# Performance work log

Hardware: AMD Instinct MI355X
Metric: run time of the kernel (lower is better)

Reference implementation:

```python
import jax, jax.numpy as jnp
import numpy as np


def setup_inputs() -> dict:
    key = jax.random.key(0)
    k1, k2, k3, k4 = jax.random.split(key, 4)
    n, C, t, h, w = 1, 256, 8, 64, 64
    heads = 8
    S = t + h + w - 2  # 134 axial positions per query
    attention = jax.random.normal(k1, (n, heads * S, t, h, w), dtype=jnp.float32)
    value = jax.random.normal(k2, (n, C, t, h, w), dtype=jnp.float32)
    conv_w = jax.random.normal(k3, (C, C), dtype=jnp.float32) / np.float32(np.sqrt(C))
    conv_b = jax.random.normal(k4, (C,), dtype=jnp.float32)
    return {"attention": attention, "value": value, "conv_w": conv_w,
            "conv_b": conv_b, "num_heads": heads}


def _grid_attn_map(A, V):
    """Criss-cross axial attention aggregation.
    A: [b, t+h+w-2, t, h, w] per-query weights over the t-axis (t entries,
       self included), h-axis (h-1 entries, self excluded) and w-axis
       (w-1 entries, self excluded).
    V: [b, c, t, h, w]. Returns [b, c, t, h, w].
    """
    b, c, t, h, w = V.shape
    A_t = A[:, :t]                  # [b, t, t, h, w]
    A_h = A[:, t:t + h - 1]         # [b, h-1, t, h, w]
    A_w = A[:, t + h - 1:]          # [b, w-1, t, h, w]

    # t-axis (self included): sum over key frame s
    out = jnp.einsum('bsthw,bcshw->bcthw', A_t, V)

    # h-axis (self excluded): channel j addresses key row p = j + (j >= q).
    # Build dense [h] channel axis with a zero at p == q via a padded gather.
    zpad = jnp.zeros((b, 1, t, h, w), A.dtype)
    A_h_pad = jnp.concatenate([A_h, zpad], axis=1)  # channel h-1 is zero
    p = jnp.arange(h)[:, None]
    q = jnp.arange(h)[None, :]
    inv_h = jnp.where(p < q, p, jnp.where(p == q, h - 1, p - 1))  # [h(p), h(q)]
    A_h_full = jnp.take_along_axis(A_h_pad, inv_h[None, :, None, :, None], axis=1)  # [b,p,t,q,w]
    out = out + jnp.einsum('bptqw,bctpw->bctqw', A_h_full, V)

    # w-axis (self excluded), same trick along w
    A_w_pad = jnp.concatenate([A_w, zpad], axis=1)  # channel w-1 is zero (h==w here OK; recompute pad generally)
    pw = jnp.arange(w)[:, None]
    qw = jnp.arange(w)[None, :]
    inv_w = jnp.where(pw < qw, pw, jnp.where(pw == qw, w - 1, pw - 1))  # [w(p), w(q)]
    A_w_full = jnp.take_along_axis(A_w_pad, inv_w[None, :, None, None, :], axis=1)  # [b,p,t,h,q]
    out = out + jnp.einsum('bpthq,bcthp->bcthq', A_w_full, V)
    return out


def reference(attention, value, conv_w, conv_b, num_heads):
    n, C, t, h, w = value.shape
    S = t + h + w - 2
    # 1x1x1 Conv3d == per-position channel matmul
    pv = jnp.einsum('ncthw,oc->nothw', value, conv_w) + conv_b[None, :, None, None, None]
    pv = pv.reshape(n * num_heads, C // num_heads, t, h, w)
    A = attention.reshape(n * num_heads, S, t, h, w)
    out = _grid_attn_map(A, pv)
    return out.reshape(n, num_heads, C // num_heads, t, h, w)
```

## Files before the change

### kernel.cpp

```cpp
#include <hip/hip_runtime.h>

#define SS   134
#define HWP  4096
#define THW  32768

typedef float f32x4 __attribute__((ext_vector_type(4)));
typedef short bf16x8 __attribute__((ext_vector_type(8)));
typedef short bf16x4 __attribute__((ext_vector_type(4)));

__device__ __forceinline__ unsigned short f2bf(float f) {
  unsigned int u = __float_as_uint(f);
  u += 0x7fff + ((u >> 16) & 1);
  return (unsigned short)(u >> 16);
}

__global__ __launch_bounds__(256) void w2bf(const float* __restrict__ W,
                                            unsigned short* __restrict__ Wbf) {
  const int i = (blockIdx.x * 256 + threadIdx.x) * 4;
  const float4 w4 = *(const float4*)&W[i];
  bf16x4 b;
  b.x = (short)f2bf(w4.x);
  b.y = (short)f2bf(w4.y);
  b.z = (short)f2bf(w4.z);
  b.w = (short)f2bf(w4.w);
  *(bf16x4*)&Wbf[i] = b;
}

__global__ __launch_bounds__(512) void conv1x1_v4(
    const float* __restrict__ V, const unsigned short* __restrict__ Wbf,
    const float* __restrict__ bias, float* __restrict__ PV) {
  __shared__ unsigned short sW[256 * 260];
  __shared__ unsigned short sV[2][128 * 40];
  const int tid = threadIdx.x;
  const int x0 = blockIdx.x * 128;
  const int lane = tid & 63;
  const int wv = tid >> 6;
  const int m = lane & 15;
  const int q = lane >> 4;

  {
    const int o = tid >> 1;
    const int half = (tid & 1) * 128;
#pragma unroll
    for (int r = 0; r < 16; ++r)
      *(bf16x8*)&sW[o * 260 + half + r * 8] =
          *(const bf16x8*)&Wbf[o * 256 + half + r * 8];
  }

  const int c_s = tid >> 4;
  const int x8 = (tid & 15) * 8;
  const float* __restrict__ vstage = V + (size_t)c_s * THW + x0 + x8;

  {
    const float4 va = *(const float4*)&vstage[0];
    const float4 vb = *(const float4*)&vstage[4];
    sV[0][(x8 + 0) * 40 + c_s] = f2bf(va.x);
    sV[0][(x8 + 1) * 40 + c_s] = f2bf(va.y);
    sV[0][(x8 + 2) * 40 + c_s] = f2bf(va.z);
    sV[0][(x8 + 3) * 40 + c_s] = f2bf(va.w);
    sV[0][(x8 + 4) * 40 + c_s] = f2bf(vb.x);
    sV[0][(x8 + 5) * 40 + c_s] = f2bf(vb.y);
    sV[0][(x8 + 6) * 40 + c_s] = f2bf(vb.z);
    sV[0][(x8 + 7) * 40 + c_s] = f2bf(vb.w);
  }
  __syncthreads();

  f32x4 acc[2][8];
#pragma unroll
  for (int i = 0; i < 2; ++i)
#pragma unroll
    for (int j = 0; j < 8; ++j)
      acc[i][j] = (f32x4){0.f, 0.f, 0.f, 0.f};

  for (int kk = 0; kk < 8; ++kk) {
    const int cur = kk & 1;
    float4 pva, pvb;
    if (kk < 7) {
      pva = *(const float4*)&vstage[(size_t)(kk + 1) * 32 * THW];
      pvb = *(const float4*)&vstage[(size_t)(kk + 1) * 32 * THW + 4];
    }
    bf16x8 fa[2], fb[8];
#pragma unroll
    for (int i = 0; i < 2; ++i)
      fa[i] = *(const bf16x8*)&sW[(wv * 32 + i * 16 + m) * 260 + kk * 32 + q * 8];
#pragma unroll
    for (int j = 0; j < 8; ++j)
      fb[j] = *(const bf16x8*)&sV[cur][(j * 16 + m) * 40 + q * 8];
#pragma unroll
    for (int i = 0; i < 2; ++i)
#pragma unroll
      for (int j = 0; j < 8; ++j)
        acc[i][j] = __builtin_amdgcn_mfma_f32_16x16x32_bf16(fa[i], fb[j], acc[i][j], 0, 0, 0);
    if (kk < 7) {
      const int nb = cur ^ 1;
      sV[nb][(x8 + 0) * 40 + c_s] = f2bf(pva.x);
      sV[nb][(x8 + 1) * 40 + c_s] = f2bf(pva.y);
      sV[nb][(x8 + 2) * 40 + c_s] = f2bf(pva.z);
      sV[nb][(x8 + 3) * 40 + c_s] = f2bf(pva.w);
      sV[nb][(x8 + 4) * 40 + c_s] = f2bf(pvb.x);
      sV[nb][(x8 + 5) * 40 + c_s] = f2bf(pvb.y);
      sV[nb][(x8 + 6) * 40 + c_s] = f2bf(pvb.z);
      sV[nb][(x8 + 7) * 40 + c_s] = f2bf(pvb.w);
    }
    __syncthreads();
  }

#pragma unroll
  for (int i = 0; i < 2; ++i) {
#pragma unroll
    for (int r = 0; r < 4; ++r) {
      const int o = wv * 32 + i * 16 + q * 4 + r;
      const float bo = bias[o];
#pragma unroll
      for (int j = 0; j < 8; ++j)
        PV[(size_t)o * THW + x0 + j * 16 + m] = acc[i][j][r] + bo;
    }
  }
}

__global__ __launch_bounds__(256) void attn_t(
    const float* __restrict__ A, const float* __restrict__ PV,
    float* __restrict__ O) {
  const int b = blockIdx.x;
  const int hd = b & 7;
  const int cb = (b >> 3) & 3;
  const int xt = b >> 5;
  const int tid = threadIdx.x;
  const int xi = xt * 128 + (tid & 31) * 4;
  const int c = cb * 8 + (tid >> 5);

  const float* __restrict__ At = A + (size_t)hd * SS * THW + xi;
  const size_t pvh = (size_t)hd * 32 * THW;
  const float* __restrict__ pvc = PV + pvh + (size_t)c * THW + xi;

  f32x4 acc[8];
#pragma unroll
  for (int t = 0; t < 8; ++t) acc[t] = (f32x4){0.f, 0.f, 0.f, 0.f};

  for (int s = 0; s < 8; ++s) {
    const f32x4 pvv = *(const f32x4*)&pvc[(size_t)s * HWP];
#pragma unroll
    for (int t = 0; t < 8; ++t) {
      const f32x4 a = *(const f32x4*)&At[(size_t)s * THW + (size_t)t * HWP];
      acc[t] += a * pvv;
    }
  }

#pragma unroll
  for (int t = 0; t < 8; ++t)
    *(f32x4*)&O[pvh + (size_t)c * THW + (size_t)t * HWP + xi] = acc[t];
}

__global__ __launch_bounds__(512) void attn_h(
    const float* __restrict__ A, const float* __restrict__ PV,
    float* __restrict__ O) {
  const int b = blockIdx.x;
  const int hd = b & 7;
  const int chb = (b >> 3) & 1;
  const int qb = (b >> 4) & 3;
  const int tq = b >> 6;
  const int tid = threadIdx.x;
  const int lane = tid & 63;
  const int wv = tid >> 6;
  const int w4 = (lane & 15) * 4;
  const int cl = lane >> 4;
  const int q0 = qb * 16 + wv * 2;
  const int c0 = chb * 16;

  __shared__ float slab[2][4 * 16 * 64];

  const float* __restrict__ Ab = A + (size_t)hd * SS * THW + (size_t)tq * HWP;
  const size_t pvh = (size_t)hd * 32 * THW;
  const float* __restrict__ PVh = PV + pvh;

  f32x4 acc[2][4];
#pragma unroll
  for (int qi = 0; qi < 2; ++qi) {
    const int q = q0 + qi;
#pragma unroll
    for (int g = 0; g < 4; ++g) {
      const int c = c0 + g * 4 + cl;
      acc[qi][g] =
          *(const f32x4*)&O[pvh + (size_t)c * THW + (size_t)tq * HWP + q * 64 + w4];
    }
  }

  const int w4s = (tid & 15) * 4;
  const int c_s = (tid >> 4) & 15;
  const int pp0 = tid >> 8;
  const float* __restrict__ pvstage =
      PVh + (size_t)(c0 + c_s) * THW + (size_t)tq * HWP + w4s;
  const int sbase = c_s * 64 + w4s;

  f32x4 stg[2];
#pragma unroll
  for (int r = 0; r < 2; ++r)
    stg[r] = *(const f32x4*)&pvstage[(pp0 + 2 * r) * 64];
#pragma unroll
  for (int r = 0; r < 2; ++r)
    *(f32x4*)&slab[0][(pp0 + 2 * r) * 1024 + sbase] = stg[r];
  __syncthreads();

  for (int ck = 0; ck < 16; ++ck) {
    const int cur = ck & 1;
    if (ck < 15) {
#pragma unroll
      for (int r = 0; r < 2; ++r)
        stg[r] = *(const f32x4*)&pvstage[((ck + 1) * 4 + pp0 + 2 * r) * 64];
    }
#pragma unroll
    for (int pp = 0; pp < 4; ++pp) {
      const int p = ck * 4 + pp;
      f32x4 a[2];
#pragma unroll
      for (int qi = 0; qi < 2; ++qi) {
        const int q = q0 + qi;
        const int row = p - (q < p ? 1 : 0);
        f32x4 av = *(const f32x4*)&Ab[(size_t)(8 + row) * THW + q * 64 + w4];
        if (q == p) av = (f32x4){0.f, 0.f, 0.f, 0.f};
        a[qi] = av;
      }
      f32x4 v[4];
#pragma unroll
      for (int g = 0; g < 4; ++g)
        v[g] = *(const f32x4*)&slab[cur][pp * 1024 + (g * 4 + cl) * 64 + w4];
#pragma unroll
      for (int qi = 0; qi < 2; ++qi)
#pragma unroll
        for (int g = 0; g < 4; ++g)
          acc[qi][g] += a[qi] * v[g];
    }
    if (ck < 15) {
#pragma unroll
      for (int r = 0; r < 2; ++r)
        *(f32x4*)&slab[cur ^ 1][(pp0 + 2 * r) * 1024 + sbase] = stg[r];
    }
    __syncthreads();
  }

#pragma unroll
  for (int qi = 0; qi < 2; ++qi) {
    const int q = q0 + qi;
#pragma unroll
    for (int g = 0; g < 4; ++g) {
      const int c = c0 + g * 4 + cl;
      *(f32x4*)&O[pvh + (size_t)c * THW + (size_t)tq * HWP + q * 64 + w4] =
          acc[qi][g];
    }
  }
}

__global__ __launch_bounds__(256) void attn_w(
    const float* __restrict__ A, const float* __restrict__ PV,
    float* __restrict__ O) {
  const int b = blockIdx.x;
  const int hb = b & 15;
  const int tq = (b >> 4) & 7;
  const int hd = b >> 7;
  const int tid = threadIdx.x;
  const int wq = tid & 63;
  const int cg = tid >> 6;
  const int h0 = hb * 4;

  __shared__ float slab[32 * 64 * 4];

  const float* __restrict__ Ab = A + (size_t)hd * SS * THW + (size_t)tq * HWP;
  const size_t pvh = (size_t)hd * 32 * THW;

#pragma unroll 4
  for (int i = 0; i < 8; ++i) {
    const int fid = tid + i * 256;
    const int w4s = (fid & 15) * 4;
    const int h = (fid >> 4) & 3;
    const int c = fid >> 6;
    const f32x4 v =
        *(const f32x4*)&PV[pvh + (size_t)c * THW + (size_t)tq * HWP + (h0 + h) * 64 + w4s];
    slab[(c * 64 + w4s + 0) * 4 + h] = v.x;
    slab[(c * 64 + w4s + 1) * 4 + h] = v.y;
    slab[(c * 64 + w4s + 2) * 4 + h] = v.z;
    slab[(c * 64 + w4s + 3) * 4 + h] = v.w;
  }

  f32x4 racc[8];
#pragma unroll
  for (int ci = 0; ci < 8; ++ci) {
    const int c = cg + ci * 4;
    f32x4 r;
#pragma unroll
    for (int hh = 0; hh < 4; ++hh)
      r[hh] = O[pvh + (size_t)c * THW + (size_t)tq * HWP + (h0 + hh) * 64 + wq];
    racc[ci] = r;
  }
  __syncthreads();

#pragma unroll 4
  for (int p = 0; p < 64; ++p) {
    const int row = 71 + p - (wq <= p ? 1 : 0);
    const float* pa = Ab + (size_t)row * THW + h0 * 64 + wq;
    f32x4 a;
    a.x = pa[0];
    a.y = pa[64];
    a.z = pa[128];
    a.w = pa[192];
    if (p == wq) a = (f32x4){0.f, 0.f, 0.f, 0.f};
#pragma unroll
    for (int ci = 0; ci < 8; ++ci) {
      const f32x4 v = *(const f32x4*)&slab[(cg + ci * 4) * 256 + p * 4];
      racc[ci] += a * v;
    }
  }

#pragma unroll
  for (int ci = 0; ci < 8; ++ci) {
    const int c = cg + ci * 4;
#pragma unroll
    for (int hh = 0; hh < 4; ++hh)
      O[pvh + (size_t)c * THW + (size_t)tq * HWP + (h0 + hh) * 64 + wq] = racc[ci][hh];
  }
}

extern "C" void kernel_launch(void* const* d_in, const int* in_sizes, int n_in,
                              void* d_out, int out_size, void* d_ws, size_t ws_size,
                              hipStream_t stream) {
  const float* A = (const float*)d_in[0];
  const float* V = (const float*)d_in[1];
  const float* W = (const float*)d_in[2];
  const float* bias = (const float*)d_in[3];
  float* out = (float*)d_out;
  float* pv = (float*)d_ws;

  unsigned short* Wbf = (unsigned short*)d_out;

  w2bf<<<dim3(64), 256, 0, stream>>>(W, Wbf);
  conv1x1_v4<<<dim3(256), 512, 0, stream>>>(V, Wbf, bias, pv);
  attn_t<<<dim3(1024), 256, 0, stream>>>(A, pv, out);
  attn_h<<<dim3(512), 512, 0, stream>>>(A, pv, out);
  attn_w<<<dim3(1024), 256, 0, stream>>>(A, pv, out);
}
```

Before: 326.9 us.

## Fuse t-axis attention into h-axis kernel and split w-kernel channels

Removes the separate attn_t kernel and folds the t-axis accumulation into the h-axis kernel, which now starts from zero instead of reloading partial output. This removes one launch and a full write-then-read round trip of the output tensor. The w-axis kernel is also split into two channel halves per block, which doubles the grid and halves the shared slab and register accumulators. The cost is that each half re-reads the same w-axis attention weights, doubling that traffic unless it hits in cache.

New measurement: 362.8 us. 1.11x slower.

```diff
diff --git a/kernel.cpp b/kernel.cpp
--- a/kernel.cpp
+++ b/kernel.cpp
@@ -118,40 +118,7 @@
   }
 }
 
-__global__ __launch_bounds__(256) void attn_t(
-    const float* __restrict__ A, const float* __restrict__ PV,
-    float* __restrict__ O) {
-  const int b = blockIdx.x;
-  const int hd = b & 7;
-  const int cb = (b >> 3) & 3;
-  const int xt = b >> 5;
-  const int tid = threadIdx.x;
-  const int xi = xt * 128 + (tid & 31) * 4;
-  const int c = cb * 8 + (tid >> 5);
-
-  const float* __restrict__ At = A + (size_t)hd * SS * THW + xi;
-  const size_t pvh = (size_t)hd * 32 * THW;
-  const float* __restrict__ pvc = PV + pvh + (size_t)c * THW + xi;
-
-  f32x4 acc[8];
-#pragma unroll
-  for (int t = 0; t < 8; ++t) acc[t] = (f32x4){0.f, 0.f, 0.f, 0.f};
-
-  for (int s = 0; s < 8; ++s) {
-    const f32x4 pvv = *(const f32x4*)&pvc[(size_t)s * HWP];
-#pragma unroll
-    for (int t = 0; t < 8; ++t) {
-      const f32x4 a = *(const f32x4*)&At[(size_t)s * THW + (size_t)t * HWP];
-      acc[t] += a * pvv;
-    }
-  }
-
-#pragma unroll
-  for (int t = 0; t < 8; ++t)
-    *(f32x4*)&O[pvh + (size_t)c * THW + (size_t)t * HWP + xi] = acc[t];
-}
-
-__global__ __launch_bounds__(512) void attn_h(
+__global__ __launch_bounds__(512) void attn_th2(
     const float* __restrict__ A, const float* __restrict__ PV,
     float* __restrict__ O) {
   const int b = blockIdx.x;
@@ -175,15 +142,10 @@
 
   f32x4 acc[2][4];
 #pragma unroll
-  for (int qi = 0; qi < 2; ++qi) {
-    const int q = q0 + qi;
-#pragma unroll
-    for (int g = 0; g < 4; ++g) {
-      const int c = c0 + g * 4 + cl;
-      acc[qi][g] =
-          *(const f32x4*)&O[pvh + (size_t)c * THW + (size_t)tq * HWP + q * 64 + w4];
-    }
-  }
+  for (int qi = 0; qi < 2; ++qi)
+#pragma unroll
+    for (int g = 0; g < 4; ++g)
+      acc[qi][g] = (f32x4){0.f, 0.f, 0.f, 0.f};
 
   const int w4s = (tid & 15) * 4;
   const int c_s = (tid >> 4) & 15;
@@ -196,6 +158,22 @@
 #pragma unroll
   for (int r = 0; r < 2; ++r)
     stg[r] = *(const f32x4*)&pvstage[(pp0 + 2 * r) * 64];
+
+  for (int s = 0; s < 8; ++s) {
+#pragma unroll
+    for (int qi = 0; qi < 2; ++qi) {
+      const int q = q0 + qi;
+      const f32x4 a = *(const f32x4*)&Ab[(size_t)s * THW + q * 64 + w4];
+#pragma unroll
+      for (int g = 0; g < 4; ++g) {
+        const int c = c0 + g * 4 + cl;
+        const f32x4 v =
+            *(const f32x4*)&PVh[(size_t)c * THW + (size_t)s * HWP + q * 64 + w4];
+        acc[qi][g] += a * v;
+      }
+    }
+  }
+
 #pragma unroll
   for (int r = 0; r < 2; ++r)
     *(f32x4*)&slab[0][(pp0 + 2 * r) * 1024 + sbase] = stg[r];
@@ -255,36 +233,38 @@
     float* __restrict__ O) {
   const int b = blockIdx.x;
   const int hb = b & 15;
-  const int tq = (b >> 4) & 7;
-  const int hd = b >> 7;
+  const int cw = (b >> 4) & 1;
+  const int tq = (b >> 5) & 7;
+  const int hd = b >> 8;
   const int tid = threadIdx.x;
   const int wq = tid & 63;
   const int cg = tid >> 6;
   const int h0 = hb * 4;
-
-  __shared__ float slab[32 * 64 * 4];
+  const int c0 = cw * 16;
+
+  __shared__ float slab[16 * 64 * 4];
 
   const float* __restrict__ Ab = A + (size_t)hd * SS * THW + (size_t)tq * HWP;
   const size_t pvh = (size_t)hd * 32 * THW;
 
-#pragma unroll 4
-  for (int i = 0; i < 8; ++i) {
+#pragma unroll
+  for (int i = 0; i < 4; ++i) {
     const int fid = tid + i * 256;
     const int w4s = (fid & 15) * 4;
     const int h = (fid >> 4) & 3;
     const int c = fid >> 6;
     const f32x4 v =
-        *(const f32x4*)&PV[pvh + (size_t)c * THW + (size_t)tq * HWP + (h0 + h) * 64 + w4s];
+        *(const f32x4*)&PV[pvh + (size_t)(c0 + c) * THW + (size_t)tq * HWP + (h0 + h) * 64 + w4s];
     slab[(c * 64 + w4s + 0) * 4 + h] = v.x;
     slab[(c * 64 + w4s + 1) * 4 + h] = v.y;
     slab[(c * 64 + w4s + 2) * 4 + h] = v.z;
     slab[(c * 64 + w4s + 3) * 4 + h] = v.w;
   }
 
-  f32x4 racc[8];
-#pragma unroll
-  for (int ci = 0; ci < 8; ++ci) {
-    const int c = cg + ci * 4;
+  f32x4 racc[4];
+#pragma unroll
+  for (int ci = 0; ci < 4; ++ci) {
+    const int c = c0 + cg + ci * 4;
     f32x4 r;
 #pragma unroll
     for (int hh = 0; hh < 4; ++hh)
@@ -304,15 +284,15 @@
     a.w = pa[192];
     if (p == wq) a = (f32x4){0.f, 0.f, 0.f, 0.f};
 #pragma unroll
-    for (int ci = 0; ci < 8; ++ci) {
+    for (int ci = 0; ci < 4; ++ci) {
       const f32x4 v = *(const f32x4*)&slab[(cg + ci * 4) * 256 + p * 4];
       racc[ci] += a * v;
     }
   }
 
 #pragma unroll
-  for (int ci = 0; ci < 8; ++ci) {
-    const int c = cg + ci * 4;
+  for (int ci = 0; ci < 4; ++ci) {
+    const int c = c0 + cg + ci * 4;
 #pragma unroll
     for (int hh = 0; hh < 4; ++hh)
       O[pvh + (size_t)c * THW + (size_t)tq * HWP + (h0 + hh) * 64 + wq] = racc[ci][hh];
@@ -333,7 +313,6 @@
 
   w2bf<<<dim3(64), 256, 0, stream>>>(W, Wbf);
   conv1x1_v4<<<dim3(256), 512, 0, stream>>>(V, Wbf, bias, pv);
-  attn_t<<<dim3(1024), 256, 0, stream>>>(A, pv, out);
-  attn_h<<<dim3(512), 512, 0, stream>>>(A, pv, out);
-  attn_w<<<dim3(1024), 256, 0, stream>>>(A, pv, out);
-}
+  attn_th2<<<dim3(512), 512, 0, stream>>>(A, pv, out);
+  attn_w<<<dim3(2048), 256, 0, stream>>>(A, pv, out);
+}
```

## Pre-convert V to bf16 in a fused cast kernel and split attn_w over channels

Applied to the files above, without the earlier changes.

A single cast kernel now converts both V and W to bf16, writing them into the output buffer as scratch. The conv kernel then loads 8 bf16 values per thread instead of converting fp32 in its inner loop. Separately, attn_w is split into two channel halves, doubling its grid and halving its shared slab and register accumulators to raise occupancy. The cost is an extra full pass over V in memory, and every attn_w block now re-reads its attention rows once per channel half.

Measured after the change: 347.4 us. +6.3%, slower.

```diff
diff --git a/kernel.cpp b/kernel.cpp
--- a/kernel.cpp
+++ b/kernel.cpp
@@ -14,20 +14,33 @@
   return (unsigned short)(u >> 16);
 }
 
-__global__ __launch_bounds__(256) void w2bf(const float* __restrict__ W,
-                                            unsigned short* __restrict__ Wbf) {
-  const int i = (blockIdx.x * 256 + threadIdx.x) * 4;
-  const float4 w4 = *(const float4*)&W[i];
-  bf16x4 b;
-  b.x = (short)f2bf(w4.x);
-  b.y = (short)f2bf(w4.y);
-  b.z = (short)f2bf(w4.z);
-  b.w = (short)f2bf(w4.w);
-  *(bf16x4*)&Wbf[i] = b;
-}
-
-__global__ __launch_bounds__(512) void conv1x1_v4(
-    const float* __restrict__ V, const unsigned short* __restrict__ Wbf,
+__global__ __launch_bounds__(256) void inputs_bf(
+    const float* __restrict__ V, const float* __restrict__ W,
+    unsigned short* __restrict__ Vbf, unsigned short* __restrict__ Wbf) {
+  const int b = blockIdx.x;
+  if (b < 8192) {
+    const int i = b * 1024 + threadIdx.x * 4;
+    const float4 v4 = *(const float4*)&V[i];
+    bf16x4 o;
+    o.x = (short)f2bf(v4.x);
+    o.y = (short)f2bf(v4.y);
+    o.z = (short)f2bf(v4.z);
+    o.w = (short)f2bf(v4.w);
+    *(bf16x4*)&Vbf[i] = o;
+  } else {
+    const int i = (b - 8192) * 1024 + threadIdx.x * 4;
+    const float4 w4 = *(const float4*)&W[i];
+    bf16x4 o;
+    o.x = (short)f2bf(w4.x);
+    o.y = (short)f2bf(w4.y);
+    o.z = (short)f2bf(w4.z);
+    o.w = (short)f2bf(w4.w);
+    *(bf16x4*)&Wbf[i] = o;
+  }
+}
+
+__global__ __launch_bounds__(512) void conv1x1_v5(
+    const unsigned short* __restrict__ Vbf, const unsigned short* __restrict__ Wbf,
     const float* __restrict__ bias, float* __restrict__ PV) {
   __shared__ unsigned short sW[256 * 260];
   __shared__ unsigned short sV[2][128 * 40];
@@ -49,19 +62,13 @@
 
   const int c_s = tid >> 4;
   const int x8 = (tid & 15) * 8;
-  const float* __restrict__ vstage = V + (size_t)c_s * THW + x0 + x8;
+  const unsigned short* __restrict__ vstage = Vbf + (size_t)c_s * THW + x0 + x8;
 
   {
-    const float4 va = *(const float4*)&vstage[0];
-    const float4 vb = *(const float4*)&vstage[4];
-    sV[0][(x8 + 0) * 40 + c_s] = f2bf(va.x);
-    sV[0][(x8 + 1) * 40 + c_s] = f2bf(va.y);
-    sV[0][(x8 + 2) * 40 + c_s] = f2bf(va.z);
-    sV[0][(x8 + 3) * 40 + c_s] = f2bf(va.w);
-    sV[0][(x8 + 4) * 40 + c_s] = f2bf(vb.x);
-    sV[0][(x8 + 5) * 40 + c_s] = f2bf(vb.y);
-    sV[0][(x8 + 6) * 40 + c_s] = f2bf(vb.z);
-    sV[0][(x8 + 7) * 40 + c_s] = f2bf(vb.w);
+    const bf16x8 v8 = *(const bf16x8*)&vstage[0];
+#pragma unroll
+    for (int e = 0; e < 8; ++e)
+      sV[0][(x8 + e) * 40 + c_s] = (unsigned short)v8[e];
   }
   __syncthreads();
 
@@ -74,10 +81,9 @@
 
   for (int kk = 0; kk < 8; ++kk) {
     const int cur = kk & 1;
-    float4 pva, pvb;
+    bf16x8 pv8;
     if (kk < 7) {
-      pva = *(const float4*)&vstage[(size_t)(kk + 1) * 32 * THW];
-      pvb = *(const float4*)&vstage[(size_t)(kk + 1) * 32 * THW + 4];
+      pv8 = *(const bf16x8*)&vstage[(size_t)(kk + 1) * 32 * THW];
     }
     bf16x8 fa[2], fb[8];
 #pragma unroll
@@ -93,14 +99,9 @@
         acc[i][j] = __builtin_amdgcn_mfma_f32_16x16x32_bf16(fa[i], fb[j], acc[i][j], 0, 0, 0);
     if (kk < 7) {
       const int nb = cur ^ 1;
-      sV[nb][(x8 + 0) * 40 + c_s] = f2bf(pva.x);
-      sV[nb][(x8 + 1) * 40 + c_s] = f2bf(pva.y);
-      sV[nb][(x8 + 2) * 40 + c_s] = f2bf(pva.z);
-      sV[nb][(x8 + 3) * 40 + c_s] = f2bf(pva.w);
-      sV[nb][(x8 + 4) * 40 + c_s] = f2bf(pvb.x);
-      sV[nb][(x8 + 5) * 40 + c_s] = f2bf(pvb.y);
-      sV[nb][(x8 + 6) * 40 + c_s] = f2bf(pvb.z);
-      sV[nb][(x8 + 7) * 40 + c_s] = f2bf(pvb.w);
+#pragma unroll
+      for (int e = 0; e < 8; ++e)
+        sV[nb][(x8 + e) * 40 + c_s] = (unsigned short)pv8[e];
     }
     __syncthreads();
   }
@@ -255,36 +256,38 @@
     float* __restrict__ O) {
   const int b = blockIdx.x;
   const int hb = b & 15;
-  const int tq = (b >> 4) & 7;
-  const int hd = b >> 7;
+  const int cw = (b >> 4) & 1;
+  const int tq = (b >> 5) & 7;
+  const int hd = b >> 8;
   const int tid = threadIdx.x;
   const int wq = tid & 63;
   const int cg = tid >> 6;
   const int h0 = hb * 4;
-
-  __shared__ float slab[32 * 64 * 4];
+  const int c0 = cw * 16;
+
+  __shared__ float slab[16 * 64 * 4];
 
   const float* __restrict__ Ab = A + (size_t)hd * SS * THW + (size_t)tq * HWP;
   const size_t pvh = (size_t)hd * 32 * THW;
 
-#pragma unroll 4
-  for (int i = 0; i < 8; ++i) {
+#pragma unroll
+  for (int i = 0; i < 4; ++i) {
     const int fid = tid + i * 256;
     const int w4s = (fid & 15) * 4;
     const int h = (fid >> 4) & 3;
     const int c = fid >> 6;
     const f32x4 v =
-        *(const f32x4*)&PV[pvh + (size_t)c * THW + (size_t)tq * HWP + (h0 + h) * 64 + w4s];
+        *(const f32x4*)&PV[pvh + (size_t)(c0 + c) * THW + (size_t)tq * HWP + (h0 + h) * 64 + w4s];
     slab[(c * 64 + w4s + 0) * 4 + h] = v.x;
     slab[(c * 64 + w4s + 1) * 4 + h] = v.y;
     slab[(c * 64 + w4s + 2) * 4 + h] = v.z;
     slab[(c * 64 + w4s + 3) * 4 + h] = v.w;
   }
 
-  f32x4 racc[8];
-#pragma unroll
-  for (int ci = 0; ci < 8; ++ci) {
-    const int c = cg + ci * 4;
+  f32x4 racc[4];
+#pragma unroll
+  for (int ci = 0; ci < 4; ++ci) {
+    const int c = c0 + cg + ci * 4;
     f32x4 r;
 #pragma unroll
     for (int hh = 0; hh < 4; ++hh)
@@ -304,15 +307,15 @@
     a.w = pa[192];
     if (p == wq) a = (f32x4){0.f, 0.f, 0.f, 0.f};
 #pragma unroll
-    for (int ci = 0; ci < 8; ++ci) {
+    for (int ci = 0; ci < 4; ++ci) {
       const f32x4 v = *(const f32x4*)&slab[(cg + ci * 4) * 256 + p * 4];
       racc[ci] += a * v;
     }
   }
 
 #pragma unroll
-  for (int ci = 0; ci < 8; ++ci) {
-    const int c = cg + ci * 4;
+  for (int ci = 0; ci < 4; ++ci) {
+    const int c = c0 + cg + ci * 4;
 #pragma unroll
     for (int hh = 0; hh < 4; ++hh)
       O[pvh + (size_t)c * THW + (size_t)tq * HWP + (h0 + hh) * 64 + wq] = racc[ci][hh];
@@ -329,11 +332,12 @@
   float* out = (float*)d_out;
   float* pv = (float*)d_ws;
 
-  unsigned short* Wbf = (unsigned short*)d_out;
-
-  w2bf<<<dim3(64), 256, 0, stream>>>(W, Wbf);
-  conv1x1_v4<<<dim3(256), 512, 0, stream>>>(V, Wbf, bias, pv);
+  unsigned short* Vbf = (unsigned short*)d_out;
+  unsigned short* Wbf = Vbf + (size_t)8 * 1024 * 1024;
+
+  inputs_bf<<<dim3(8256), 256, 0, stream>>>(V, W, Vbf, Wbf);
+  conv1x1_v5<<<dim3(256), 512, 0, stream>>>(Vbf, Wbf, bias, pv);
   attn_t<<<dim3(1024), 256, 0, stream>>>(A, pv, out);
   attn_h<<<dim3(512), 512, 0, stream>>>(A, pv, out);
-  attn_w<<<dim3(1024), 256, 0, stream>>>(A, pv, out);
-}
+  attn_w<<<dim3(2048), 256, 0, stream>>>(A, pv, out);
+}
```

## Fuse t-axis aggregation into w-axis kernel and drop separate attn_t pass

Applied to the files above, without the earlier changes.

The t-axis einsum is folded into the w-axis kernel. Each block first accumulates the t contribution in registers, using the same spatial tile it already owns, then adds the w-axis terms from its shared-memory PV slab. The separate attn_t launch goes away, and so does the w kernel's read-modify-write of O, which removes one full pass of output traffic over memory. In exchange, kernel ordering changes so that attn_h now runs after the fused kernel and must accumulate into O correctly. The t-part PV loads also become scalar strided loads rather than float4 loads.

Result: no change. 329.2 us (+0.7%).

```diff
diff --git a/kernel.cpp b/kernel.cpp
--- a/kernel.cpp
+++ b/kernel.cpp
@@ -118,37 +118,86 @@
   }
 }
 
-__global__ __launch_bounds__(256) void attn_t(
+__global__ __launch_bounds__(256) void attn_tw(
     const float* __restrict__ A, const float* __restrict__ PV,
     float* __restrict__ O) {
   const int b = blockIdx.x;
-  const int hd = b & 7;
-  const int cb = (b >> 3) & 3;
-  const int xt = b >> 5;
+  const int hb = b & 15;
+  const int tq = (b >> 4) & 7;
+  const int hd = b >> 7;
   const int tid = threadIdx.x;
-  const int xi = xt * 128 + (tid & 31) * 4;
-  const int c = cb * 8 + (tid >> 5);
-
-  const float* __restrict__ At = A + (size_t)hd * SS * THW + xi;
+  const int wq = tid & 63;
+  const int cg = tid >> 6;
+  const int h0 = hb * 4;
+
+  __shared__ float slab[32 * 64 * 4];
+
+  const float* __restrict__ Ab = A + (size_t)hd * SS * THW + (size_t)tq * HWP;
   const size_t pvh = (size_t)hd * 32 * THW;
-  const float* __restrict__ pvc = PV + pvh + (size_t)c * THW + xi;
-
-  f32x4 acc[8];
-#pragma unroll
-  for (int t = 0; t < 8; ++t) acc[t] = (f32x4){0.f, 0.f, 0.f, 0.f};
+
+#pragma unroll
+  for (int i = 0; i < 8; ++i) {
+    const int fid = tid + i * 256;
+    const int w4s = (fid & 15) * 4;
+    const int h = (fid >> 4) & 3;
+    const int c = fid >> 6;
+    const f32x4 v =
+        *(const f32x4*)&PV[pvh + (size_t)c * THW + (size_t)tq * HWP + (h0 + h) * 64 + w4s];
+    slab[(c * 64 + w4s + 0) * 4 + h] = v.x;
+    slab[(c * 64 + w4s + 1) * 4 + h] = v.y;
+    slab[(c * 64 + w4s + 2) * 4 + h] = v.z;
+    slab[(c * 64 + w4s + 3) * 4 + h] = v.w;
+  }
+
+  f32x4 racc[8];
+#pragma unroll
+  for (int ci = 0; ci < 8; ++ci) racc[ci] = (f32x4){0.f, 0.f, 0.f, 0.f};
 
   for (int s = 0; s < 8; ++s) {
-    const f32x4 pvv = *(const f32x4*)&pvc[(size_t)s * HWP];
-#pragma unroll
-    for (int t = 0; t < 8; ++t) {
-      const f32x4 a = *(const f32x4*)&At[(size_t)s * THW + (size_t)t * HWP];
-      acc[t] += a * pvv;
-    }
-  }
-
-#pragma unroll
-  for (int t = 0; t < 8; ++t)
-    *(f32x4*)&O[pvh + (size_t)c * THW + (size_t)t * HWP + xi] = acc[t];
+    const float* pa = Ab + (size_t)s * THW + h0 * 64 + wq;
+    f32x4 a;
+    a.x = pa[0];
+    a.y = pa[64];
+    a.z = pa[128];
+    a.w = pa[192];
+#pragma unroll
+    for (int ci = 0; ci < 8; ++ci) {
+      const int c = cg + ci * 4;
+      const float* pp = &PV[pvh + (size_t)c * THW + (size_t)s * HWP + h0 * 64 + wq];
+      f32x4 v;
+      v.x = pp[0];
+      v.y = pp[64];
+      v.z = pp[128];
+      v.w = pp[192];
+      racc[ci] += a * v;
+    }
+  }
+  __syncthreads();
+
+#pragma unroll 4
+  for (int p = 0; p < 64; ++p) {
+    const int row = 71 + p - (wq <= p ? 1 : 0);
+    const float* pa = Ab + (size_t)row * THW + h0 * 64 + wq;
+    f32x4 a;
+    a.x = pa[0];
+    a.y = pa[64];
+    a.z = pa[128];
+    a.w = pa[192];
+    if (p == wq) a = (f32x4){0.f, 0.f, 0.f, 0.f};
+#pragma unroll
+    for (int ci = 0; ci < 8; ++ci) {
+      const f32x4 v = *(const f32x4*)&slab[(cg + ci * 4) * 256 + p * 4];
+      racc[ci] += a * v;
+    }
+  }
+
+#pragma unroll
+  for (int ci = 0; ci < 8; ++ci) {
+    const int c = cg + ci * 4;
+#pragma unroll
+    for (int hh = 0; hh < 4; ++hh)
+      O[pvh + (size_t)c * THW + (size_t)tq * HWP + (h0 + hh) * 64 + wq] = racc[ci][hh];
+  }
 }
 
 __global__ __launch_bounds__(512) void attn_h(
@@ -250,75 +299,6 @@
   }
 }
 
-__global__ __launch_bounds__(256) void attn_w(
-    const float* __restrict__ A, const float* __restrict__ PV,
-    float* __restrict__ O) {
-  const int b = blockIdx.x;
-  const int hb = b & 15;
-  const int tq = (b >> 4) & 7;
-  const int hd = b >> 7;
-  const int tid = threadIdx.x;
-  const int wq = tid & 63;
-  const int cg = tid >> 6;
-  const int h0 = hb * 4;
-
-  __shared__ float slab[32 * 64 * 4];
-
-  const float* __restrict__ Ab = A + (size_t)hd * SS * THW + (size_t)tq * HWP;
-  const size_t pvh = (size_t)hd * 32 * THW;
-
-#pragma unroll 4
-  for (int i = 0; i < 8; ++i) {
-    const int fid = tid + i * 256;
-    const int w4s = (fid & 15) * 4;
-    const int h = (fid >> 4) & 3;
-    const int c = fid >> 6;
-    const f32x4 v =
-        *(const f32x4*)&PV[pvh + (size_t)c * THW + (size_t)tq * HWP + (h0 + h) * 64 + w4s];
-    slab[(c * 64 + w4s + 0) * 4 + h] = v.x;
-    slab[(c * 64 + w4s + 1) * 4 + h] = v.y;
-    slab[(c * 64 + w4s + 2) * 4 + h] = v.z;
-    slab[(c * 64 + w4s + 3) * 4 + h] = v.w;
-  }
-
-  f32x4 racc[8];
-#pragma unroll
-  for (int ci = 0; ci < 8; ++ci) {
-    const int c = cg + ci * 4;
-    f32x4 r;
-#pragma unroll
-    for (int hh = 0; hh < 4; ++hh)
-      r[hh] = O[pvh + (size_t)c * THW + (size_t)tq * HWP + (h0 + hh) * 64 + wq];
-    racc[ci] = r;
-  }
-  __syncthreads();
-
-#pragma unroll 4
-  for (int p = 0; p < 64; ++p) {
-    const int row = 71 + p - (wq <= p ? 1 : 0);
-    const float* pa = Ab + (size_t)row * THW + h0 * 64 + wq;
-    f32x4 a;
-    a.x = pa[0];
-    a.y = pa[64];
-    a.z = pa[128];
-    a.w = pa[192];
-    if (p == wq) a = (f32x4){0.f, 0.f, 0.f, 0.f};
-#pragma unroll
-    for (int ci = 0; ci < 8; ++ci) {
-      const f32x4 v = *(const f32x4*)&slab[(cg + ci * 4) * 256 + p * 4];
-      racc[ci] += a * v;
-    }
-  }
-
-#pragma unroll
-  for (int ci = 0; ci < 8; ++ci) {
-    const int c = cg + ci * 4;
-#pragma unroll
-    for (int hh = 0; hh < 4; ++hh)
-      O[pvh + (size_t)c * THW + (size_t)tq * HWP + (h0 + hh) * 64 + wq] = racc[ci][hh];
-  }
-}
-
 extern "C" void kernel_launch(void* const* d_in, const int* in_sizes, int n_in,
                               void* d_out, int out_size, void* d_ws, size_t ws_size,
                               hipStream_t stream) {
@@ -333,7 +313,6 @@
 
   w2bf<<<dim3(64), 256, 0, stream>>>(W, Wbf);
   conv1x1_v4<<<dim3(256), 512, 0, stream>>>(V, Wbf, bias, pv);
-  attn_t<<<dim3(1024), 256, 0, stream>>>(A, pv, out);
+  attn_tw<<<dim3(1024), 256, 0, stream>>>(A, pv, out);
   attn_h<<<dim3(512), 512, 0, stream>>>(A, pv, out);
-  attn_w<<<dim3(1024), 256, 0, stream>>>(A, pv, out);
-}
+}
```
